# Performance work log

Hardware: AMD Instinct MI355X
Metric: run time of the kernel (lower is better)

## Reference

```python
import jax, jax.numpy as jnp
import numpy as np

N_HEAD = 100000   # head (dst/src-type) nodes
N_TAIL = 100000   # concatenated tail nodes over all edge types
E = 1600000       # total edges (avg degree 16)
IN = 128          # in_features_len (node_feature_hid_len)
OUT = 32          # out_features_len (GAT_hid_len)
NHEAD = 4
EDGE_FEATS = 32
N_ETYPES = 8
SLOPE = 0.2       # leakyrelu negative_slope


def _uniform_reset(k, shape, fan_in, fan_out):
    stdv = np.sqrt(6.0 / (fan_in + fan_out)).astype(np.float32)
    return jax.random.uniform(k, shape, jnp.float32, -stdv, stdv)


def setup_inputs() -> dict:
    key = jax.random.key(0)
    ks = jax.random.split(key, 10)
    return {
        "head_feature": jax.random.normal(ks[0], (N_HEAD, IN), jnp.float32),
        "tail_feature": jax.random.normal(ks[1], (N_TAIL, IN), jnp.float32),
        "edge_list": jax.random.randint(ks[2], (2, E), 0, N_HEAD, jnp.int32),
        "tmp_edge": jax.random.randint(ks[3], (E,), 0, N_ETYPES, jnp.int32),
        "W": _uniform_reset(ks[4], (IN, OUT * NHEAD), IN, OUT * NHEAD),
        "W_e": _uniform_reset(ks[5], (EDGE_FEATS, EDGE_FEATS * NHEAD), EDGE_FEATS, EDGE_FEATS * NHEAD),
        "a_l": _uniform_reset(ks[6], (1, NHEAD, OUT), NHEAD, OUT),
        "a_r": _uniform_reset(ks[7], (1, NHEAD, OUT), NHEAD, OUT),
        "a_e": _uniform_reset(ks[8], (1, NHEAD, EDGE_FEATS), NHEAD, EDGE_FEATS),
        "edge_emb": _uniform_reset(ks[9], (N_ETYPES, EDGE_FEATS), N_ETYPES, EDGE_FEATS),
    }


def reference(head_feature, tail_feature, edge_list, tmp_edge, W, W_e, a_l, a_r, a_e, edge_emb):
    # SimpleHGNLayer.forward (eval mode: dropouts are identity; res_attn=None;
    # first layer => node_residual=None; activation=elu).
    h_head = (head_feature @ W).reshape(-1, NHEAD, OUT)   # [N_head, H, D]
    h_tail = (tail_feature @ W).reshape(-1, NHEAD, OUT)   # [N_tail, H, D]
    e = (edge_emb @ W_e).reshape(-1, NHEAD, EDGE_FEATS)   # [T, H, De]

    head_ind = edge_list[0]
    tail_ind = edge_list[1]

    h_l = (a_l * h_head).sum(-1)[head_ind]                # [E, H]
    h_r = (a_r * h_tail).sum(-1)[tail_ind]                # [E, H]
    h_e = (a_e * e).sum(-1)[tmp_edge]                     # [E, H]
    att = jax.nn.leaky_relu(h_l + h_r + h_e, SLOPE)       # [E, H]

    # torch.sparse.softmax(dim=1) == softmax over edges sharing a head node
    m = jax.ops.segment_max(att, head_ind, num_segments=N_HEAD)       # [N_head, H]
    att_exp = jnp.exp(att - m[head_ind])
    denom = jax.ops.segment_sum(att_exp, head_ind, num_segments=N_HEAD)
    alpha = att_exp / denom[head_ind]                     # [E, H]

    # torch.sparse.mm(attn_n, h_tail[:, n, :]) for each head, vectorized
    msg = alpha[:, :, None] * h_tail[tail_ind]            # [E, H, D]
    out = jax.ops.segment_sum(msg, head_ind, num_segments=N_HEAD)     # [N_head, H, D]
    out = out.reshape(N_HEAD, NHEAD * OUT)
    return jax.nn.elu(out)
```

## Files before the change

### kernel.cpp

```cpp
#include <hip/hip_runtime.h>
#include <hip/hip_bf16.h>
#include <hip/hip_fp16.h>
#include <math.h>

#define N_HEADN 100000
#define N_TAILN 100000
#define NEDGE   1600000
#define SLOPE   0.2f

#define NB   196
#define HPB  512
#define BCAP 9216

static __device__ __forceinline__ float bf2f(__hip_bfloat16 x) { return __bfloat162float(x); }

#define FMA_MIX_LO(acc, pk, q) \
  asm("v_fma_mix_f32 %0, %1, %2, %0 op_sel_hi:[1,0,0]" : "+v"(acc) : "v"(pk), "v"(q))
#define FMA_MIX_HI(acc, pk, q) \
  asm("v_fma_mix_f32 %0, %1, %2, %0 op_sel:[1,0,0] op_sel_hi:[1,0,0]" : "+v"(acc) : "v"(pk), "v"(q))

__global__ __launch_bounds__(256) void k0m(const float* __restrict__ W,
                                           const float* __restrict__ W_e,
                                           const float* __restrict__ a_l,
                                           const float* __restrict__ a_e,
                                           const float* __restrict__ emb,
                                           __hip_bfloat16* __restrict__ Wb,
                                           float* __restrict__ wl,
                                           float* __restrict__ he) {
  const int i = (blockIdx.x * 256 + threadIdx.x) * 4;
  const float4 v = *(const float4*)&W[i];
  union { unsigned short us[4]; uint2 u2; } pk;
  __hip_bfloat16 b0 = __float2bfloat16(v.x); pk.us[0] = *(unsigned short*)&b0;
  __hip_bfloat16 b1 = __float2bfloat16(v.y); pk.us[1] = *(unsigned short*)&b1;
  __hip_bfloat16 b2 = __float2bfloat16(v.z); pk.us[2] = *(unsigned short*)&b2;
  __hip_bfloat16 b3 = __float2bfloat16(v.w); pk.us[3] = *(unsigned short*)&b3;
  *(uint2*)&Wb[i] = pk.u2;
  if (blockIdx.x == 0 && threadIdx.x < 128) {
    const int t = threadIdx.x;
    #pragma unroll
    for (int h = 0; h < 4; ++h) {
      float sl = 0.f;
      for (int d = 0; d < 32; ++d)
        sl += W[t * 128 + h * 32 + d] * a_l[h * 32 + d];
      wl[t * 4 + h] = sl;
    }
    if (t < 32) {
      const int et = t >> 2, h = t & 3;
      float acc = 0.f;
      for (int d = 0; d < 32; ++d) {
        float tmp = 0.f;
        for (int f = 0; f < 32; ++f)
          tmp += emb[et * 32 + f] * W_e[f * 128 + h * 32 + d];
        acc += a_e[h * 32 + d] * tmp;
      }
      he[et * 4 + h] = acc;
    }
  }
}

__global__ __launch_bounds__(256) void k1_hlr(const float* __restrict__ feat,
                                              const float* __restrict__ wv,
                                              float* __restrict__ o) {
  const int gid = blockIdx.x * 256 + threadIdx.x;
  const int node = gid >> 4, li = gid & 15;
  const float4* row = (const float4*)(feat + (size_t)node * 128 + li * 8);
  const float4 x0 = row[0], x1 = row[1];
  const float* w = wv + li * 32;
  float p0 = 0.f, p1 = 0.f, p2 = 0.f, p3 = 0.f;
  const float xs[8] = {x0.x, x0.y, x0.z, x0.w, x1.x, x1.y, x1.z, x1.w};
  #pragma unroll
  for (int j = 0; j < 8; ++j) {
    const float4 wj = *(const float4*)&w[j * 4];
    p0 += xs[j] * wj.x;
    p1 += xs[j] * wj.y;
    p2 += xs[j] * wj.z;
    p3 += xs[j] * wj.w;
  }
  #pragma unroll
  for (int m = 8; m; m >>= 1) {
    p0 += __shfl_xor(p0, m, 64);
    p1 += __shfl_xor(p1, m, 64);
    p2 += __shfl_xor(p2, m, 64);
    p3 += __shfl_xor(p3, m, 64);
  }
  if (li == 0) *(float4*)(o + (size_t)node * 4) = make_float4(p0, p1, p2, p3);
}

__global__ __launch_bounds__(256) void k2_gemm(const float* __restrict__ A,
                                               const __hip_bfloat16* __restrict__ Wb,
                                               const float* __restrict__ a_r,
                                               __half* __restrict__ out,
                                               float* __restrict__ h_r) {
  __shared__ __hip_bfloat16 sW[128 * 128];
  __shared__ __hip_bfloat16 sA[128 * 68];
  const int t = threadIdx.x;
  {
    const uint4* src = (const uint4*)Wb;
    uint4* dst = (uint4*)sW;
    #pragma unroll
    for (int i = 0; i < 8; ++i) dst[i * 256 + t] = src[i * 256 + t];
  }
  const int r0 = blockIdx.x * 64;
  #pragma unroll
  for (int ii = 0; ii < 8; ++ii) {
    const int i = ii * 256 + t;
    const int r = i >> 5, k4 = (i & 31) * 4;
    float4 v = make_float4(0.f, 0.f, 0.f, 0.f);
    if (r0 + r < N_TAILN) v = *(const float4*)&A[(size_t)(r0 + r) * 128 + k4];
    sA[(k4 + 0) * 68 + r] = __float2bfloat16(v.x);
    sA[(k4 + 1) * 68 + r] = __float2bfloat16(v.y);
    sA[(k4 + 2) * 68 + r] = __float2bfloat16(v.z);
    sA[(k4 + 3) * 68 + r] = __float2bfloat16(v.w);
  }
  __syncthreads();

  const int tc = t & 15, tr = t >> 4;
  const int c8 = tc * 8, r4 = tr * 4;
  float acc[4][8];
  #pragma unroll
  for (int i = 0; i < 4; ++i)
    #pragma unroll
    for (int j = 0; j < 8; ++j) acc[i][j] = 0.f;

  #pragma unroll 2
  for (int k = 0; k < 128; ++k) {
    const uint2 ab = *(const uint2*)&sA[k * 68 + r4];
    const float ar[4] = {__uint_as_float(ab.x << 16), __uint_as_float(ab.x & 0xffff0000u),
                         __uint_as_float(ab.y << 16), __uint_as_float(ab.y & 0xffff0000u)};
    const uint4 wbv = *(const uint4*)&sW[k * 128 + c8];
    float w[8];
    w[0] = __uint_as_float(wbv.x << 16); w[1] = __uint_as_float(wbv.x & 0xffff0000u);
    w[2] = __uint_as_float(wbv.y << 16); w[3] = __uint_as_float(wbv.y & 0xffff0000u);
    w[4] = __uint_as_float(wbv.z << 16); w[5] = __uint_as_float(wbv.z & 0xffff0000u);
    w[6] = __uint_as_float(wbv.w << 16); w[7] = __uint_as_float(wbv.w & 0xffff0000u);
    #pragma unroll
    for (int i = 0; i < 4; ++i)
      #pragma unroll
      for (int j = 0; j < 8; ++j)
        acc[i][j] += ar[i] * w[j];
  }

  const int hh = tc >> 2, d0 = (tc & 3) * 8;
  const float4 ar0 = *(const float4*)&a_r[hh * 32 + d0];
  const float4 ar1 = *(const float4*)&a_r[hh * 32 + d0 + 4];
  #pragma unroll
  for (int i = 0; i < 4; ++i) {
    float hr = acc[i][0] * ar0.x + acc[i][1] * ar0.y + acc[i][2] * ar0.z + acc[i][3] * ar0.w
             + acc[i][4] * ar1.x + acc[i][5] * ar1.y + acc[i][6] * ar1.z + acc[i][7] * ar1.w;
    hr += __shfl_xor(hr, 1, 64);
    hr += __shfl_xor(hr, 2, 64);
    if ((tc & 3) == 0 && (r0 + r4 + i) < N_TAILN)
      h_r[(size_t)(r0 + r4 + i) * 4 + hh] = hr;
  }

  #pragma unroll
  for (int i = 0; i < 4; ++i) {
    const int rr = r0 + r4 + i;
    if (rr < N_TAILN) {
      union { unsigned short us[8]; uint4 u4; } pk;
      #pragma unroll
      for (int j = 0; j < 8; ++j) {
        __half b = __float2half(acc[i][j]);
        pk.us[j] = *(unsigned short*)&b;
      }
      *(uint4*)&out[(size_t)rr * 128 + c8] = pk.u4;
    }
  }
}

__global__ __launch_bounds__(256) void p1_part(const int* __restrict__ head_ind,
                                               const int* __restrict__ tail_ind,
                                               const int* __restrict__ etype,
                                               int* __restrict__ bucketCursor,
                                               unsigned int* __restrict__ recs) {
  __shared__ int hist[NB];
  const int t = threadIdx.x;
  for (int i = t; i < NB; i += 256) hist[i] = 0;
  __syncthreads();
  const int e0 = blockIdx.x * 1280;
  int h[5];
  #pragma unroll
  for (int i = 0; i < 5; ++i) {
    h[i] = head_ind[e0 + i * 256 + t];
    atomicAdd(&hist[h[i] >> 9], 1);
  }
  __syncthreads();
  for (int i = t; i < NB; i += 256) {
    const int c = hist[i];
    hist[i] = (c > 0) ? atomicAdd(&bucketCursor[i], c) : 0;
  }
  __syncthreads();
  #pragma unroll
  for (int i = 0; i < 5; ++i) {
    const int e = e0 + i * 256 + t;
    const int hi = h[i];
    const int b = hi >> 9;
    const int pos = atomicAdd(&hist[b], 1);
    recs[b * BCAP + pos] = (unsigned)tail_ind[e] | ((unsigned)etype[e] << 17)
                         | ((unsigned)(hi & 511) << 20);
  }
}

__global__ __launch_bounds__(1024) void p23(const unsigned int* __restrict__ recs,
                                            const int* __restrict__ bucketCursor,
                                            int* __restrict__ off,
                                            int* __restrict__ pt) {
  __shared__ int cur[HPB];
  __shared__ int red[256];
  const int b = blockIdx.x, t = threadIdx.x;
  if (t < 256) red[t] = (t < b) ? bucketCursor[t] : 0;
  if (t < HPB) cur[t] = 0;
  __syncthreads();
  for (int st = 128; st; st >>= 1) {
    if (t < st) red[t] += red[t + st];
    __syncthreads();
  }
  const int bstart = red[0];
  const int cnt = bucketCursor[b];
  const unsigned int* __restrict__ rb = recs + (size_t)b * BCAP;
  for (int i = t; i < cnt; i += 1024)
    atomicAdd(&cur[rb[i] >> 20], 1);
  __syncthreads();
  const int orig = (t < HPB) ? cur[t] : 0;
  for (int st = 1; st < HPB; st <<= 1) {
    int v = 0;
    if (t < HPB && t >= st) v = cur[t - st];
    __syncthreads();
    if (t < HPB) cur[t] += v;
    __syncthreads();
  }
  const int h0 = b * HPB;
  if (t < HPB) {
    const int excl = bstart + cur[t] - orig;
    cur[t] = excl;
    if (h0 + t < N_HEADN) off[h0 + t] = excl;
  }
  if (b == NB - 1 && t == 0) off[N_HEADN] = NEDGE;
  __syncthreads();
  for (int i = t; i < cnt; i += 1024) {
    const unsigned r = rb[i];
    const int pos = atomicAdd(&cur[r >> 20], 1);
    pt[pos] = (int)(r & 0xFFFFFu);
  }
}

__global__ __launch_bounds__(256) void k4_agg(const int* __restrict__ off,
                                              const int* __restrict__ pt,
                                              const float* __restrict__ h_l,
                                              const float* __restrict__ h_r,
                                              const float* __restrict__ he,
                                              const __half* __restrict__ h_tail,
                                              float* __restrict__ out) {
  __shared__ __align__(16) float sw[4][4][72];
  __shared__ int sti[4][4][20];
  __shared__ __align__(16) float4 she4[8];
  const int wid = threadIdx.x >> 6;
  const int lane = threadIdx.x & 63;
  const int g = lane >> 4, li = lane & 15;
  if (threadIdx.x < 8) she4[threadIdx.x] = ((const float4*)he)[threadIdx.x];
  __syncthreads();
  const int n = blockIdx.x * 16 + wid * 4 + g;
  const int s = off[n], e = off[n + 1];
  const int nch = (e - s + 15) >> 4;
  const float4 hl = *(const float4*)(h_l + (size_t)n * 4);
  const int h = li >> 2;
  const unsigned dby = (unsigned)li * 16u;
  float m0 = -1e30f, m1 = -1e30f, m2 = -1e30f, m3 = -1e30f;
  float s0 = 0.f, s1 = 0.f, s2 = 0.f, s3 = 0.f;
  float acc[8];
  #pragma unroll
  for (int d = 0; d < 8; ++d) acc[d] = 0.f;
  float* __restrict__ swg = &sw[wid][g][0];
  int* __restrict__ stig = &sti[wid][g][0];
  const char* __restrict__ htb = (const char*)h_tail;
  for (int c = 0; c < nch; ++c) {
    const int base = s + (c << 4);
    const int rem = min(16, e - base);
    float a0 = -1e30f, a1 = -1e30f, a2 = -1e30f, a3 = -1e30f;
    if (li < rem) {
      const int pk = pt[base + li];
      const unsigned ti = (unsigned)pk & 0x1FFFFu;
      const int et = (pk >> 17) & 7;
      const float4 hr = *(const float4*)((const char*)h_r + (ti << 4));
      const float4 hv = she4[et];
      a0 = hl.x + hr.x + hv.x;
      a1 = hl.y + hr.y + hv.y;
      a2 = hl.z + hr.z + hv.z;
      a3 = hl.w + hr.w + hv.w;
      a0 = fmaxf(a0, SLOPE * a0);
      a1 = fmaxf(a1, SLOPE * a1);
      a2 = fmaxf(a2, SLOPE * a2);
      a3 = fmaxf(a3, SLOPE * a3);
      stig[li] = (int)(ti << 8);
    }
    float c0 = a0, c1 = a1, c2 = a2, c3 = a3;
    #pragma unroll
    for (int msk = 8; msk; msk >>= 1) {
      c0 = fmaxf(c0, __shfl_xor(c0, msk, 64));
      c1 = fmaxf(c1, __shfl_xor(c1, msk, 64));
      c2 = fmaxf(c2, __shfl_xor(c2, msk, 64));
      c3 = fmaxf(c3, __shfl_xor(c3, msk, 64));
    }
    const float nm0 = fmaxf(m0, c0), nm1 = fmaxf(m1, c1);
    const float nm2 = fmaxf(m2, c2), nm3 = fmaxf(m3, c3);
    const float e0 = __expf(m0 - nm0), e1 = __expf(m1 - nm1);
    const float e2 = __expf(m2 - nm2), e3 = __expf(m3 - nm3);
    const float w0 = __expf(a0 - nm0), w1 = __expf(a1 - nm1);
    const float w2 = __expf(a2 - nm2), w3 = __expf(a3 - nm3);
    float t0 = w0, t1 = w1, t2 = w2, t3 = w3;
    #pragma unroll
    for (int msk = 8; msk; msk >>= 1) {
      t0 += __shfl_xor(t0, msk, 64);
      t1 += __shfl_xor(t1, msk, 64);
      t2 += __shfl_xor(t2, msk, 64);
      t3 += __shfl_xor(t3, msk, 64);
    }
    s0 = s0 * e0 + t0; s1 = s1 * e1 + t1;
    s2 = s2 * e2 + t2; s3 = s3 * e3 + t3;
    m0 = nm0; m1 = nm1; m2 = nm2; m3 = nm3;
    *(float4*)&swg[li * 4] = make_float4(w0, w1, w2, w3);
    const float sc = (h == 0) ? e0 : (h == 1) ? e1 : (h == 2) ? e2 : e3;
    #pragma unroll
    for (int d = 0; d < 8; ++d) acc[d] *= sc;
    __builtin_amdgcn_wave_barrier();
    int j = 0;
    for (; j + 4 <= rem; j += 4) {
      const int o0 = stig[j], o1 = stig[j + 1], o2 = stig[j + 2], o3 = stig[j + 3];
      const float q0 = swg[(j + 0) * 4 + h];
      const float q1 = swg[(j + 1) * 4 + h];
      const float q2 = swg[(j + 2) * 4 + h];
      const float q3 = swg[(j + 3) * 4 + h];
      const uint4 v0 = *(const uint4*)(htb + (unsigned)o0 + dby);
      const uint4 v1 = *(const uint4*)(htb + (unsigned)o1 + dby);
      const uint4 v2 = *(const uint4*)(htb + (unsigned)o2 + dby);
      const uint4 v3 = *(const uint4*)(htb + (unsigned)o3 + dby);
      FMA_MIX_LO(acc[0], v0.x, q0); FMA_MIX_HI(acc[1], v0.x, q0);
      FMA_MIX_LO(acc[2], v0.y, q0); FMA_MIX_HI(acc[3], v0.y, q0);
      FMA_MIX_LO(acc[4], v0.z, q0); FMA_MIX_HI(acc[5], v0.z, q0);
      FMA_MIX_LO(acc[6], v0.w, q0); FMA_MIX_HI(acc[7], v0.w, q0);
      FMA_MIX_LO(acc[0], v1.x, q1); FMA_MIX_HI(acc[1], v1.x, q1);
      FMA_MIX_LO(acc[2], v1.y, q1); FMA_MIX_HI(acc[3], v1.y, q1);
      FMA_MIX_LO(acc[4], v1.z, q1); FMA_MIX_HI(acc[5], v1.z, q1);
      FMA_MIX_LO(acc[6], v1.w, q1); FMA_MIX_HI(acc[7], v1.w, q1);
      FMA_MIX_LO(acc[0], v2.x, q2); FMA_MIX_HI(acc[1], v2.x, q2);
      FMA_MIX_LO(acc[2], v2.y, q2); FMA_MIX_HI(acc[3], v2.y, q2);
      FMA_MIX_LO(acc[4], v2.z, q2); FMA_MIX_HI(acc[5], v2.z, q2);
      FMA_MIX_LO(acc[6], v2.w, q2); FMA_MIX_HI(acc[7], v2.w, q2);
      FMA_MIX_LO(acc[0], v3.x, q3); FMA_MIX_HI(acc[1], v3.x, q3);
      FMA_MIX_LO(acc[2], v3.y, q3); FMA_MIX_HI(acc[3], v3.y, q3);
      FMA_MIX_LO(acc[4], v3.z, q3); FMA_MIX_HI(acc[5], v3.z, q3);
      FMA_MIX_LO(acc[6], v3.w, q3); FMA_MIX_HI(acc[7], v3.w, q3);
    }
    for (; j < rem; ++j) {
      const int o = stig[j];
      const float q = swg[j * 4 + h];
      const uint4 v = *(const uint4*)(htb + (unsigned)o + dby);
      FMA_MIX_LO(acc[0], v.x, q); FMA_MIX_HI(acc[1], v.x, q);
      FMA_MIX_LO(acc[2], v.y, q); FMA_MIX_HI(acc[3], v.y, q);
      FMA_MIX_LO(acc[4], v.z, q); FMA_MIX_HI(acc[5], v.z, q);
      FMA_MIX_LO(acc[6], v.w, q); FMA_MIX_HI(acc[7], v.w, q);
    }
    __builtin_amdgcn_wave_barrier();
  }
  const float denom = (h == 0) ? s0 : (h == 1) ? s1 : (h == 2) ? s2 : s3;
  const float inv = denom > 0.f ? 1.f / denom : 0.f;
  float o[8];
  #pragma unroll
  for (int d = 0; d < 8; ++d) {
    const float v = acc[d] * inv;
    o[d] = v > 0.f ? v : expm1f(v);
  }
  float* op = out + (size_t)n * 128 + li * 8;
  *(float4*)op = make_float4(o[0], o[1], o[2], o[3]);
  *(float4*)(op + 4) = make_float4(o[4], o[5], o[6], o[7]);
}

extern "C" void kernel_launch(void* const* d_in, const int* in_sizes, int n_in,
                              void* d_out, int out_size, void* d_ws, size_t ws_size,
                              hipStream_t stream) {
  const float* head = (const float*)d_in[0];
  const float* tail = (const float*)d_in[1];
  const int* elist  = (const int*)d_in[2];
  const int* etype  = (const int*)d_in[3];
  const float* W    = (const float*)d_in[4];
  const float* W_e  = (const float*)d_in[5];
  const float* a_l  = (const float*)d_in[6];
  const float* a_r  = (const float*)d_in[7];
  const float* a_e  = (const float*)d_in[8];
  const float* emb  = (const float*)d_in[9];
  const int* head_ind = elist;
  const int* tail_ind = elist + NEDGE;
  (void)in_sizes; (void)n_in; (void)out_size; (void)ws_size;

  char* p = (char*)d_ws;
  size_t o = 0;
  auto carve = [&](size_t bytes) {
    char* r = p + o;
    o += (bytes + 255) & ~(size_t)255;
    return r;
  };
  __half* h_tail = (__half*)carve((size_t)N_TAILN * 128 * 2);
  int*   pt     = (int*)   carve((size_t)NEDGE * 4);
  unsigned int* recs = (unsigned int*)carve((size_t)NB * BCAP * 4);
  float* h_l    = (float*) carve((size_t)N_HEADN * 4 * 4);
  float* h_r    = (float*) carve((size_t)N_TAILN * 4 * 4);
  int*   off    = (int*)   carve((size_t)(N_HEADN + 1) * 4);
  int*   bucketCursor = (int*)carve(NB * 4);
  float* wl     = (float*) carve(128 * 4 * 4);
  float* he     = (float*) carve(8 * 4 * 4);
  __hip_bfloat16* Wb = (__hip_bfloat16*)carve(16384 * 2);

  hipMemsetAsync(bucketCursor, 0, NB * sizeof(int), stream);
  k0m<<<16, 256, 0, stream>>>(W, W_e, a_l, a_e, emb, Wb, wl, he);
  k1_hlr<<<(N_HEADN * 16) / 256, 256, 0, stream>>>(head, wl, h_l);
  k2_gemm<<<(N_TAILN + 63) / 64, 256, 0, stream>>>(tail, Wb, a_r, h_tail, h_r);
  p1_part<<<NEDGE / 1280, 256, 0, stream>>>(head_ind, tail_ind, etype, bucketCursor, recs);
  p23<<<NB, 1024, 0, stream>>>(recs, bucketCursor, off, pt);
  k4_agg<<<N_HEADN / 16, 256, 0, stream>>>(off, pt, h_l, h_r, he, h_tail, (float*)d_out);
}
```

Baseline: 364.4 us.

## Use MFMA bf16 matrix instructions for the tail feature projection GEMM

Rewrites the tail-feature GEMM to use 16x16x32 bf16 MFMA instructions instead of scalar FMA over shared-memory tiles. A is loaded straight from global memory into fragments, and W is pre-transposed to bf16 in the setup kernel so B fragments can be read from padded shared memory. The h_r attention projection is recomputed from the MFMA accumulator layout using cross-lane shuffles. The output is now written as scattered 2-byte half stores, which may coalesce worse than the previous 16-byte stores.

```diff
diff --git a/kernel.cpp b/kernel.cpp
--- a/kernel.cpp
+++ b/kernel.cpp
@@ -18,23 +18,25 @@
   asm("v_fma_mix_f32 %0, %1, %2, %0 op_sel_hi:[1,0,0]" : "+v"(acc) : "v"(pk), "v"(q))
 #define FMA_MIX_HI(acc, pk, q) \
   asm("v_fma_mix_f32 %0, %1, %2, %0 op_sel:[1,0,0] op_sel_hi:[1,0,0]" : "+v"(acc) : "v"(pk), "v"(q))
+
+typedef __attribute__((ext_vector_type(8))) short bfrag;
+typedef __attribute__((ext_vector_type(4))) float ffrag;
 
 __global__ __launch_bounds__(256) void k0m(const float* __restrict__ W,
                                            const float* __restrict__ W_e,
                                            const float* __restrict__ a_l,
                                            const float* __restrict__ a_e,
                                            const float* __restrict__ emb,
-                                           __hip_bfloat16* __restrict__ Wb,
+                                           __hip_bfloat16* __restrict__ WbT,
                                            float* __restrict__ wl,
                                            float* __restrict__ he) {
   const int i = (blockIdx.x * 256 + threadIdx.x) * 4;
+  const int r = i >> 7, c = i & 127;
   const float4 v = *(const float4*)&W[i];
-  union { unsigned short us[4]; uint2 u2; } pk;
-  __hip_bfloat16 b0 = __float2bfloat16(v.x); pk.us[0] = *(unsigned short*)&b0;
-  __hip_bfloat16 b1 = __float2bfloat16(v.y); pk.us[1] = *(unsigned short*)&b1;
-  __hip_bfloat16 b2 = __float2bfloat16(v.z); pk.us[2] = *(unsigned short*)&b2;
-  __hip_bfloat16 b3 = __float2bfloat16(v.w); pk.us[3] = *(unsigned short*)&b3;
-  *(uint2*)&Wb[i] = pk.u2;
+  WbT[(size_t)(c + 0) * 128 + r] = __float2bfloat16(v.x);
+  WbT[(size_t)(c + 1) * 128 + r] = __float2bfloat16(v.y);
+  WbT[(size_t)(c + 2) * 128 + r] = __float2bfloat16(v.z);
+  WbT[(size_t)(c + 3) * 128 + r] = __float2bfloat16(v.w);
   if (blockIdx.x == 0 && threadIdx.x < 128) {
     const int t = threadIdx.x;
     #pragma unroll
@@ -87,83 +89,93 @@
 }
 
 __global__ __launch_bounds__(256) void k2_gemm(const float* __restrict__ A,
-                                               const __hip_bfloat16* __restrict__ Wb,
+                                               const __hip_bfloat16* __restrict__ WbT,
                                                const float* __restrict__ a_r,
                                                __half* __restrict__ out,
                                                float* __restrict__ h_r) {
-  __shared__ __hip_bfloat16 sW[128 * 128];
-  __shared__ __hip_bfloat16 sA[128 * 68];
+  __shared__ __hip_bfloat16 sBT[128 * 136];
+  __shared__ float sAr[128];
   const int t = threadIdx.x;
   {
-    const uint4* src = (const uint4*)Wb;
-    uint4* dst = (uint4*)sW;
-    #pragma unroll
-    for (int i = 0; i < 8; ++i) dst[i * 256 + t] = src[i * 256 + t];
-  }
-  const int r0 = blockIdx.x * 64;
-  #pragma unroll
-  for (int ii = 0; ii < 8; ++ii) {
-    const int i = ii * 256 + t;
-    const int r = i >> 5, k4 = (i & 31) * 4;
-    float4 v = make_float4(0.f, 0.f, 0.f, 0.f);
-    if (r0 + r < N_TAILN) v = *(const float4*)&A[(size_t)(r0 + r) * 128 + k4];
-    sA[(k4 + 0) * 68 + r] = __float2bfloat16(v.x);
-    sA[(k4 + 1) * 68 + r] = __float2bfloat16(v.y);
-    sA[(k4 + 2) * 68 + r] = __float2bfloat16(v.z);
-    sA[(k4 + 3) * 68 + r] = __float2bfloat16(v.w);
-  }
-  __syncthreads();
-
-  const int tc = t & 15, tr = t >> 4;
-  const int c8 = tc * 8, r4 = tr * 4;
-  float acc[4][8];
-  #pragma unroll
-  for (int i = 0; i < 4; ++i)
-    #pragma unroll
-    for (int j = 0; j < 8; ++j) acc[i][j] = 0.f;
-
-  #pragma unroll 2
-  for (int k = 0; k < 128; ++k) {
-    const uint2 ab = *(const uint2*)&sA[k * 68 + r4];
-    const float ar[4] = {__uint_as_float(ab.x << 16), __uint_as_float(ab.x & 0xffff0000u),
-                         __uint_as_float(ab.y << 16), __uint_as_float(ab.y & 0xffff0000u)};
-    const uint4 wbv = *(const uint4*)&sW[k * 128 + c8];
-    float w[8];
-    w[0] = __uint_as_float(wbv.x << 16); w[1] = __uint_as_float(wbv.x & 0xffff0000u);
-    w[2] = __uint_as_float(wbv.y << 16); w[3] = __uint_as_float(wbv.y & 0xffff0000u);
-    w[4] = __uint_as_float(wbv.z << 16); w[5] = __uint_as_float(wbv.z & 0xffff0000u);
-    w[6] = __uint_as_float(wbv.w << 16); w[7] = __uint_as_float(wbv.w & 0xffff0000u);
-    #pragma unroll
-    for (int i = 0; i < 4; ++i)
+    const uint4* src = (const uint4*)WbT;
+    #pragma unroll
+    for (int it = 0; it < 8; ++it) {
+      const int i = it * 256 + t;
+      *(uint4*)&sBT[(i >> 4) * 136 + (i & 15) * 8] = src[i];
+    }
+  }
+  if (t < 128) sAr[t] = a_r[t];
+  __syncthreads();
+
+  const int w = t >> 6, l = t & 63;
+  const int lm = l & 15, kg = l >> 4;
+  const int row = blockIdx.x * 64 + w * 16 + lm;
+  const int rowc = row < N_TAILN ? row : N_TAILN - 1;
+  const float* __restrict__ Arow = A + (size_t)rowc * 128 + kg * 8;
+
+  ffrag acc[8];
+  #pragma unroll
+  for (int nt = 0; nt < 8; ++nt) acc[nt] = (ffrag){0.f, 0.f, 0.f, 0.f};
+
+  #pragma unroll
+  for (int kc = 0; kc < 4; ++kc) {
+    const float4 va = *(const float4*)(Arow + kc * 32);
+    const float4 vb = *(const float4*)(Arow + kc * 32 + 4);
+    union { unsigned short us[8]; bfrag v; } af;
+    __hip_bfloat16 b;
+    b = __float2bfloat16(va.x); af.us[0] = *(unsigned short*)&b;
+    b = __float2bfloat16(va.y); af.us[1] = *(unsigned short*)&b;
+    b = __float2bfloat16(va.z); af.us[2] = *(unsigned short*)&b;
+    b = __float2bfloat16(va.w); af.us[3] = *(unsigned short*)&b;
+    b = __float2bfloat16(vb.x); af.us[4] = *(unsigned short*)&b;
+    b = __float2bfloat16(vb.y); af.us[5] = *(unsigned short*)&b;
+    b = __float2bfloat16(vb.z); af.us[6] = *(unsigned short*)&b;
+    b = __float2bfloat16(vb.w); af.us[7] = *(unsigned short*)&b;
+    const int kb = kc * 32 + kg * 8;
+    #pragma unroll
+    for (int nt = 0; nt < 8; ++nt) {
+      const bfrag bf = *(const bfrag*)&sBT[(nt * 16 + lm) * 136 + kb];
+      acc[nt] = __builtin_amdgcn_mfma_f32_16x16x32_bf16(af.v, bf, acc[nt], 0, 0, 0);
+    }
+  }
+
+  float ph[4][4];
+  #pragma unroll
+  for (int hh = 0; hh < 4; ++hh)
+    #pragma unroll
+    for (int i = 0; i < 4; ++i) ph[hh][i] = 0.f;
+  #pragma unroll
+  for (int nt = 0; nt < 8; ++nt) {
+    const float ar = sAr[nt * 16 + lm];
+    #pragma unroll
+    for (int i = 0; i < 4; ++i) ph[nt >> 1][i] += acc[nt][i] * ar;
+  }
+  #pragma unroll
+  for (int hh = 0; hh < 4; ++hh)
+    #pragma unroll
+    for (int i = 0; i < 4; ++i) {
+      ph[hh][i] += __shfl_xor(ph[hh][i], 1, 64);
+      ph[hh][i] += __shfl_xor(ph[hh][i], 2, 64);
+      ph[hh][i] += __shfl_xor(ph[hh][i], 4, 64);
+      ph[hh][i] += __shfl_xor(ph[hh][i], 8, 64);
+    }
+  if (lm == 0) {
+    #pragma unroll
+    for (int i = 0; i < 4; ++i) {
+      const int rr = blockIdx.x * 64 + w * 16 + kg * 4 + i;
+      if (rr < N_TAILN)
+        *(float4*)&h_r[(size_t)rr * 4] = make_float4(ph[0][i], ph[1][i], ph[2][i], ph[3][i]);
+    }
+  }
+
+  #pragma unroll
+  for (int i = 0; i < 4; ++i) {
+    const int rr = blockIdx.x * 64 + w * 16 + kg * 4 + i;
+    if (rr < N_TAILN) {
+      __half* orow = out + (size_t)rr * 128 + lm;
       #pragma unroll
-      for (int j = 0; j < 8; ++j)
-        acc[i][j] += ar[i] * w[j];
-  }
-
-  const int hh = tc >> 2, d0 = (tc & 3) * 8;
-  const float4 ar0 = *(const float4*)&a_r[hh * 32 + d0];
-  const float4 ar1 = *(const float4*)&a_r[hh * 32 + d0 + 4];
-  #pragma unroll
-  for (int i = 0; i < 4; ++i) {
-    float hr = acc[i][0] * ar0.x + acc[i][1] * ar0.y + acc[i][2] * ar0.z + acc[i][3] * ar0.w
-             + acc[i][4] * ar1.x + acc[i][5] * ar1.y + acc[i][6] * ar1.z + acc[i][7] * ar1.w;
-    hr += __shfl_xor(hr, 1, 64);
-    hr += __shfl_xor(hr, 2, 64);
-    if ((tc & 3) == 0 && (r0 + r4 + i) < N_TAILN)
-      h_r[(size_t)(r0 + r4 + i) * 4 + hh] = hr;
-  }
-
-  #pragma unroll
-  for (int i = 0; i < 4; ++i) {
-    const int rr = r0 + r4 + i;
-    if (rr < N_TAILN) {
-      union { unsigned short us[8]; uint4 u4; } pk;
-      #pragma unroll
-      for (int j = 0; j < 8; ++j) {
-        __half b = __float2half(acc[i][j]);
-        pk.us[j] = *(unsigned short*)&b;
-      }
-      *(uint4*)&out[(size_t)rr * 128 + c8] = pk.u4;
+      for (int nt = 0; nt < 8; ++nt)
+        orow[nt * 16] = __float2half(acc[nt][i]);
     }
   }
 }
@@ -408,12 +420,12 @@
   int*   bucketCursor = (int*)carve(NB * 4);
   float* wl     = (float*) carve(128 * 4 * 4);
   float* he     = (float*) carve(8 * 4 * 4);
-  __hip_bfloat16* Wb = (__hip_bfloat16*)carve(16384 * 2);
+  __hip_bfloat16* WbT = (__hip_bfloat16*)carve(16384 * 2);
 
   hipMemsetAsync(bucketCursor, 0, NB * sizeof(int), stream);
-  k0m<<<16, 256, 0, stream>>>(W, W_e, a_l, a_e, emb, Wb, wl, he);
+  k0m<<<16, 256, 0, stream>>>(W, W_e, a_l, a_e, emb, WbT, wl, he);
   k1_hlr<<<(N_HEADN * 16) / 256, 256, 0, stream>>>(head, wl, h_l);
-  k2_gemm<<<(N_TAILN + 63) / 64, 256, 0, stream>>>(tail, Wb, a_r, h_tail, h_r);
+  k2_gemm<<<(N_TAILN + 63) / 64, 256, 0, stream>>>(tail, WbT, a_r, h_tail, h_r);
   p1_part<<<NEDGE / 1280, 256, 0, stream>>>(head_ind, tail_ind, etype, bucketCursor, recs);
   p23<<<NB, 1024, 0, stream>>>(recs, bucketCursor, off, pt);
   k4_agg<<<N_HEADN / 16, 256, 0, stream>>>(off, pt, h_l, h_r, he, h_tail, (float*)d_out);
```

After: 327.2 us. 1.11x faster.
